# Kernel optimization log

Measured on AMD Instinct MI355X. Metric: run time of the kernel, lower is better.

Reference implementation:

```python
import jax, jax.numpy as jnp
import numpy as np

MARGIN = 0.2
EPS = 1e-6  # torch.pairwise_distance adds eps to the difference before the norm


def setup_inputs() -> dict:
    key = jax.random.key(0)
    k1, k2, k3 = jax.random.split(key, 3)
    B, D = 8192, 128
    emb1 = jax.random.normal(k1, (B, D), dtype=jnp.float32)
    emb2 = jax.random.normal(k2, (B, D), dtype=jnp.float32)
    target = jax.random.randint(k3, (B,), 0, 2, dtype=jnp.int64)
    return {"emb1": emb1, "emb2": emb2, "target": target}


def reference(emb1, emb2, target):
    B, D = emb1.shape
    # torch.pairwise_distance(a, b) = ||a - b + EPS||_2; expand the square:
    # |a-b+eps|^2 = |a|^2 + |b|^2 - 2 a.b + 2*eps*(sum(a)-sum(b)) + D*eps^2
    sq = (
        jnp.sum(emb1 * emb1, axis=-1)[:, None]
        + jnp.sum(emb2 * emb2, axis=-1)[None, :]
        - 2.0 * (emb1 @ emb2.T)
        + 2.0 * EPS * (jnp.sum(emb1, axis=-1)[:, None] - jnp.sum(emb2, axis=-1)[None, :])
        + D * EPS * EPS
    )
    dist = jnp.sqrt(jnp.maximum(sq, 0.0))  # [B, B]: dist[i, j] = ||emb1[i] - emb2[j] + eps||

    pos = target == 1
    neg = target == 0
    # hardest positive: max over columns j with target[j]==1; hardest negative: min over target[j]==0
    pos_max = jnp.max(jnp.where(pos[None, :], dist, -jnp.inf), axis=1)  # [B]
    neg_min = jnp.min(jnp.where(neg[None, :], dist, jnp.inf), axis=1)   # [B]
    per_anchor = jnp.maximum(pos_max - neg_min + MARGIN, 0.0)
    anchor_w = pos.astype(dist.dtype)
    # mean over anchors (rows i with target[i]==1)
    return jnp.sum(per_anchor * anchor_w) / jnp.sum(anchor_w)
```

## Files before the change

### kernel.cpp

```cpp
#include <hip/hip_runtime.h>
#include <hip/hip_bf16.h>
#include <math.h>


#define DDIM   128
#define SPLITS 8
#define MARGIN 0.2f
#define EPS    1e-6f
#define SENT   1e30f

#define CHUNK_PITCH 1056
#define WAVE_SPAN   (8 * CHUNK_PITCH)
#define TILE_BYTES  (4 * WAVE_SPAN)

typedef unsigned short ushort_t;
typedef __attribute__((ext_vector_type(8))) short short8;
typedef __attribute__((ext_vector_type(4))) float f32x4;

__device__ __forceinline__ ushort_t f2bf(float f) {
    unsigned int u = __float_as_uint(f);
    u = (u + 0x7FFFu + ((u >> 16) & 1u)) >> 16;
    return (ushort_t)u;
}

__device__ __forceinline__ void g2lds16(const ushort_t* g, void* lds) {
    __builtin_amdgcn_global_load_lds(
        (const __attribute__((address_space(1))) unsigned int*)g,
        (__attribute__((address_space(3))) unsigned int*)lds,
        16, 0, 0);
}

__global__ void prep_kernel(const float* __restrict__ e1, const float* __restrict__ e2,
                            const int* __restrict__ target,
                            ushort_t* __restrict__ e1b, ushort_t* __restrict__ e2b,
                            float* __restrict__ rowterm,
                            float* __restrict__ cpos, float* __restrict__ cneg,
                            float* __restrict__ redsum, int* __restrict__ ticket, int B) {
    if (blockIdx.x == 0 && threadIdx.x == 0) {
        redsum[0] = 0.f; redsum[1] = 0.f; *ticket = 0;
    }
    int w    = (blockIdx.x * blockDim.x + threadIdx.x) >> 6;
    int lane = threadIdx.x & 63;
    if (w >= 2 * B) return;
    bool first = (w < B);
    int r = first ? w : w - B;
    const float* src = (first ? e1 : e2) + (size_t)r * DDIM;
    float2 v = *(const float2*)(src + lane * 2);
    ushort_t* dst = (first ? e1b : e2b) + (size_t)r * DDIM;
    ushort2 o; o.x = f2bf(v.x); o.y = f2bf(v.y);
    *(ushort2*)(dst + lane * 2) = o;
    float s = v.x + v.y;
    float n = v.x * v.x + v.y * v.y;
    #pragma unroll
    for (int off = 32; off > 0; off >>= 1) {
        s += __shfl_down(s, off, 64);
        n += __shfl_down(n, off, 64);
    }
    if (lane == 0) {
        if (first) {
            rowterm[r] = n + 2.f * EPS * s + (float)DDIM * EPS * EPS;
        } else {
            float ct = n - 2.f * EPS * s;
            int tg = target[r];
            cpos[r] = (tg == 1) ? ct : -SENT;
            cneg[r] = (tg == 0) ? ct :  SENT;
        }
    }
}

__global__ __launch_bounds__(256, 2)
void tile_kernel(const ushort_t* __restrict__ e1b, const ushort_t* __restrict__ e2b,
                 const float* __restrict__ cpos, const float* __restrict__ cneg,
                 float* __restrict__ pmp, float* __restrict__ nmp, int B) {
    __shared__ __align__(16) unsigned char Bs[2][TILE_BYTES];
    __shared__ float smP[128], smN[128];

    const int tid = threadIdx.x;
    const int w   = tid >> 6;
    const int l   = tid & 63;
    const int lq  = l >> 4;
    const int lm  = l & 15;
    const int row0 = blockIdx.x * 128;
    const int colSpan = B / SPLITS;
    const int col0 = blockIdx.y * colSpan;
    const int nTiles = colSpan / 128;

    const int wr = (w >> 1) * 64;
    const int wc = (w & 1) * 64;

    auto stageB = [&](int t, int buf) {
        const ushort_t* g = e2b + (size_t)(col0 + t * 128 + w * 32) * DDIM + l * 8;
        unsigned char* lp = Bs[buf] + w * WAVE_SPAN;
        #pragma unroll
        for (int it = 0; it < 8; ++it)
            g2lds16(g + it * 512, lp + it * CHUNK_PITCH);
    };

    stageB(0, 0);

    short8 afr[4][4];
    {
        const ushort_t* aG = e1b + (size_t)(row0 + wr + lm) * DDIM + lq * 8;
        #pragma unroll
        for (int i = 0; i < 4; ++i)
            #pragma unroll
            for (int k4 = 0; k4 < 4; ++k4)
                afr[i][k4] = *(const short8*)(aG + i * 16 * DDIM + k4 * 32);
    }

    const int bOff = ((wc >> 2) + (lm >> 2)) * CHUNK_PITCH + (lm & 3) * 256 + lq * 16;

    float pm[4][4], nm[4][4];
    #pragma unroll
    for (int i = 0; i < 4; ++i)
        #pragma unroll
        for (int r = 0; r < 4; ++r) { pm[i][r] = -SENT; nm[i][r] = SENT; }

    __syncthreads();

    for (int t = 0; t < nTiles; ++t) {
        if (t + 1 < nTiles) stageB(t + 1, (t + 1) & 1);

        const unsigned char* bLane = Bs[t & 1] + bOff;

        f32x4 acc[4][4];
        #pragma unroll
        for (int i = 0; i < 4; ++i)
            #pragma unroll
            for (int j = 0; j < 4; ++j)
                acc[i][j] = (f32x4){0.f, 0.f, 0.f, 0.f};

        #pragma unroll
        for (int kk = 0; kk < DDIM; kk += 32) {
            const int k4 = kk >> 5;
            const int ko = kk * 2;
            short8 bf[4];
            #pragma unroll
            for (int j = 0; j < 4; ++j)
                bf[j] = *(const short8*)(bLane + j * (4 * CHUNK_PITCH) + ko);
            #pragma unroll
            for (int i = 0; i < 4; ++i)
                #pragma unroll
                for (int j = 0; j < 4; ++j)
                    acc[i][j] = __builtin_amdgcn_mfma_f32_16x16x32_bf16(
                                    afr[i][k4], bf[j], acc[i][j], 0, 0, 0);
        }

        #pragma unroll
        for (int j = 0; j < 4; ++j) {
            int col = col0 + t * 128 + wc + j * 16 + lm;
            float cp = cpos[col];
            float cn = cneg[col];
            #pragma unroll
            for (int i = 0; i < 4; ++i)
                #pragma unroll
                for (int r = 0; r < 4; ++r) {
                    float d = acc[i][j][r];
                    pm[i][r] = fmaxf(pm[i][r], fmaf(-2.f, d, cp));
                    nm[i][r] = fminf(nm[i][r], fmaf(-2.f, d, cn));
                }
        }

        if (t + 1 < nTiles)
            __syncthreads();
    }

    #pragma unroll
    for (int m = 1; m < 16; m <<= 1) {
        #pragma unroll
        for (int i = 0; i < 4; ++i)
            #pragma unroll
            for (int r = 0; r < 4; ++r) {
                pm[i][r] = fmaxf(pm[i][r], __shfl_xor(pm[i][r], m, 64));
                nm[i][r] = fminf(nm[i][r], __shfl_xor(nm[i][r], m, 64));
            }
    }

    __syncthreads();
    if ((w & 1) == 1 && lm == 0) {
        #pragma unroll
        for (int i = 0; i < 4; ++i)
            #pragma unroll
            for (int r = 0; r < 4; ++r) {
                int lr = wr + i * 16 + lq * 4 + r;
                smP[lr] = pm[i][r];
                smN[lr] = nm[i][r];
            }
    }
    __syncthreads();
    if ((w & 1) == 0 && lm == 0) {
        #pragma unroll
        for (int i = 0; i < 4; ++i)
            #pragma unroll
            for (int r = 0; r < 4; ++r) {
                int lr  = wr + i * 16 + lq * 4 + r;
                int row = row0 + lr;
                pmp[(size_t)blockIdx.y * B + row] = fmaxf(pm[i][r], smP[lr]);
                nmp[(size_t)blockIdx.y * B + row] = fminf(nm[i][r], smN[lr]);
            }
    }
}

__global__ void reduce_kernel(const float* __restrict__ pmp, const float* __restrict__ nmp,
                              const float* __restrict__ rowterm, const int* __restrict__ target,
                              float* __restrict__ redsum, int* __restrict__ ticket,
                              float* __restrict__ out, int B) {
    int row = blockIdx.x * blockDim.x + threadIdx.x;
    float s = 0.f, c = 0.f;
    {
        float pmv = -SENT, nmv = SENT;
        #pragma unroll
        for (int sp = 0; sp < SPLITS; ++sp) {
            pmv = fmaxf(pmv, pmp[(size_t)sp * B + row]);
            nmv = fminf(nmv, nmp[(size_t)sp * B + row]);
        }
        float rt = rowterm[row];
        float dp = sqrtf(fmaxf(rt + pmv, 0.f));
        float dn = sqrtf(fmaxf(rt + nmv, 0.f));
        if (target[row] == 1) {
            s = fmaxf(dp - dn + MARGIN, 0.f);
            c = 1.f;
        }
    }
    #pragma unroll
    for (int off = 32; off > 0; off >>= 1) {
        s += __shfl_down(s, off, 64);
        c += __shfl_down(c, off, 64);
    }
    __shared__ float ls[4], lc[4];
    int wv = threadIdx.x >> 6, ln = threadIdx.x & 63;
    if (ln == 0) { ls[wv] = s; lc[wv] = c; }
    __syncthreads();
    if (threadIdx.x == 0) {
        float ss = ls[0] + ls[1] + ls[2] + ls[3];
        float cc = lc[0] + lc[1] + lc[2] + lc[3];
        atomicAdd(&redsum[0], ss);
        atomicAdd(&redsum[1], cc);
        __threadfence();
        int done = atomicAdd(ticket, 1);
        if (done == (int)gridDim.x - 1) {
            __threadfence();
            float fs = __hip_atomic_load(&redsum[0], __ATOMIC_RELAXED, __HIP_MEMORY_SCOPE_AGENT);
            float fc = __hip_atomic_load(&redsum[1], __ATOMIC_RELAXED, __HIP_MEMORY_SCOPE_AGENT);
            out[0] = fs / fc;
        }
    }
}

extern "C" void kernel_launch(void* const* d_in, const int* in_sizes, int n_in,
                              void* d_out, int out_size, void* d_ws, size_t ws_size,
                              hipStream_t stream) {
    const float* e1     = (const float*)d_in[0];
    const float* e2     = (const float*)d_in[1];
    const int*   target = (const int*)d_in[2];
    float* out = (float*)d_out;
    const int B = in_sizes[2];

    char* p = (char*)d_ws;
    ushort_t* e1b  = (ushort_t*)p;   p += (size_t)B * DDIM * 2;
    ushort_t* e2b  = (ushort_t*)p;   p += (size_t)B * DDIM * 2;
    float* rowterm = (float*)p;      p += (size_t)B * 4;
    float* cpos    = (float*)p;      p += (size_t)B * 4;
    float* cneg    = (float*)p;      p += (size_t)B * 4;
    float* pmp     = (float*)p;      p += (size_t)SPLITS * B * 4;
    float* nmp     = (float*)p;      p += (size_t)SPLITS * B * 4;
    float* redsum  = (float*)p;      p += 2 * 4;
    int*   ticket  = (int*)p;

    {
        int blocks = (2 * B + 3) / 4;
        prep_kernel<<<blocks, 256, 0, stream>>>(e1, e2, target, e1b, e2b,
                                                rowterm, cpos, cneg, redsum, ticket, B);
    }
    {
        dim3 grid(B / 128, SPLITS);
        tile_kernel<<<grid, 256, 0, stream>>>(e1b, e2b, cpos, cneg, pmp, nmp, B);
    }
    reduce_kernel<<<32, 256, 0, stream>>>(pmp, nmp, rowterm, target,
                                          redsum, ticket, out, B);
}
```

Measured before the change: 92.09 us.

## Fuse final reduction into tile kernel via atomic max keys and last-block ticket

Replaces the per-split partial max/min buffers and separate reduce kernel with order-preserving uint-encoded atomicMax updates per row, then lets the last finishing tile block compute the final loss. This removes one kernel launch and the partial-buffer round trip. It adds global atomics per row, a serial single-block final reduction over all B rows, and fences in every block.

```diff
diff --git a/kernel.cpp b/kernel.cpp
--- a/kernel.cpp
+++ b/kernel.cpp
@@ -23,6 +23,15 @@
     return (ushort_t)u;
 }
 
+__device__ __forceinline__ unsigned enc(float f) {
+    unsigned b = __float_as_uint(f);
+    return (b & 0x80000000u) ? ~b : (b | 0x80000000u);
+}
+__device__ __forceinline__ float dec(unsigned k) {
+    unsigned b = (k & 0x80000000u) ? (k & 0x7FFFFFFFu) : ~k;
+    return __uint_as_float(b);
+}
+
 __device__ __forceinline__ void g2lds16(const ushort_t* g, void* lds) {
     __builtin_amdgcn_global_load_lds(
         (const __attribute__((address_space(1))) unsigned int*)g,
@@ -35,11 +44,13 @@
                             ushort_t* __restrict__ e1b, ushort_t* __restrict__ e2b,
                             float* __restrict__ rowterm,
                             float* __restrict__ cpos, float* __restrict__ cneg,
-                            float* __restrict__ redsum, int* __restrict__ ticket, int B) {
-    if (blockIdx.x == 0 && threadIdx.x == 0) {
-        redsum[0] = 0.f; redsum[1] = 0.f; *ticket = 0;
-    }
-    int w    = (blockIdx.x * blockDim.x + threadIdx.x) >> 6;
+                            unsigned* __restrict__ pmkey, unsigned* __restrict__ nmkey,
+                            int* __restrict__ ticket, int B) {
+    int gtid = blockIdx.x * blockDim.x + threadIdx.x;
+    if (gtid < B) { pmkey[gtid] = 0u; nmkey[gtid] = 0u; }
+    if (gtid == 0) *ticket = 0;
+
+    int w    = gtid >> 6;
     int lane = threadIdx.x & 63;
     if (w >= 2 * B) return;
     bool first = (w < B);
@@ -71,9 +82,12 @@
 __global__ __launch_bounds__(256, 2)
 void tile_kernel(const ushort_t* __restrict__ e1b, const ushort_t* __restrict__ e2b,
                  const float* __restrict__ cpos, const float* __restrict__ cneg,
-                 float* __restrict__ pmp, float* __restrict__ nmp, int B) {
-    __shared__ __align__(16) unsigned char Bs[2][TILE_BYTES];
+                 const float* __restrict__ rowterm, const int* __restrict__ target,
+                 unsigned* __restrict__ pmkey, unsigned* __restrict__ nmkey,
+                 int* __restrict__ ticket, float* __restrict__ out, int B) {
+    __shared__ __align__(16) unsigned char Bsm[2][TILE_BYTES];
     __shared__ float smP[128], smN[128];
+    __shared__ int lastSh;
 
     const int tid = threadIdx.x;
     const int w   = tid >> 6;
@@ -84,13 +98,14 @@
     const int colSpan = B / SPLITS;
     const int col0 = blockIdx.y * colSpan;
     const int nTiles = colSpan / 128;
+    const int nBlocks = gridDim.x * gridDim.y;
 
     const int wr = (w >> 1) * 64;
     const int wc = (w & 1) * 64;
 
     auto stageB = [&](int t, int buf) {
         const ushort_t* g = e2b + (size_t)(col0 + t * 128 + w * 32) * DDIM + l * 8;
-        unsigned char* lp = Bs[buf] + w * WAVE_SPAN;
+        unsigned char* lp = Bsm[buf] + w * WAVE_SPAN;
         #pragma unroll
         for (int it = 0; it < 8; ++it)
             g2lds16(g + it * 512, lp + it * CHUNK_PITCH);
@@ -121,7 +136,7 @@
     for (int t = 0; t < nTiles; ++t) {
         if (t + 1 < nTiles) stageB(t + 1, (t + 1) & 1);
 
-        const unsigned char* bLane = Bs[t & 1] + bOff;
+        const unsigned char* bLane = Bsm[t & 1] + bOff;
 
         f32x4 acc[4][4];
         #pragma unroll
@@ -161,8 +176,7 @@
                 }
         }
 
-        if (t + 1 < nTiles)
-            __syncthreads();
+        if (t + 1 < nTiles) __syncthreads();
     }
 
     #pragma unroll
@@ -195,55 +209,48 @@
             for (int r = 0; r < 4; ++r) {
                 int lr  = wr + i * 16 + lq * 4 + r;
                 int row = row0 + lr;
-                pmp[(size_t)blockIdx.y * B + row] = fmaxf(pm[i][r], smP[lr]);
-                nmp[(size_t)blockIdx.y * B + row] = fminf(nm[i][r], smN[lr]);
-            }
-    }
-}
-
-__global__ void reduce_kernel(const float* __restrict__ pmp, const float* __restrict__ nmp,
-                              const float* __restrict__ rowterm, const int* __restrict__ target,
-                              float* __restrict__ redsum, int* __restrict__ ticket,
-                              float* __restrict__ out, int B) {
-    int row = blockIdx.x * blockDim.x + threadIdx.x;
-    float s = 0.f, c = 0.f;
-    {
-        float pmv = -SENT, nmv = SENT;
-        #pragma unroll
-        for (int sp = 0; sp < SPLITS; ++sp) {
-            pmv = fmaxf(pmv, pmp[(size_t)sp * B + row]);
-            nmv = fminf(nmv, nmp[(size_t)sp * B + row]);
-        }
-        float rt = rowterm[row];
-        float dp = sqrtf(fmaxf(rt + pmv, 0.f));
-        float dn = sqrtf(fmaxf(rt + nmv, 0.f));
-        if (target[row] == 1) {
-            s = fmaxf(dp - dn + MARGIN, 0.f);
-            c = 1.f;
-        }
-    }
-    #pragma unroll
-    for (int off = 32; off > 0; off >>= 1) {
-        s += __shfl_down(s, off, 64);
-        c += __shfl_down(c, off, 64);
-    }
-    __shared__ float ls[4], lc[4];
-    int wv = threadIdx.x >> 6, ln = threadIdx.x & 63;
-    if (ln == 0) { ls[wv] = s; lc[wv] = c; }
-    __syncthreads();
-    if (threadIdx.x == 0) {
-        float ss = ls[0] + ls[1] + ls[2] + ls[3];
-        float cc = lc[0] + lc[1] + lc[2] + lc[3];
-        atomicAdd(&redsum[0], ss);
-        atomicAdd(&redsum[1], cc);
+                float p = fmaxf(pm[i][r], smP[lr]);
+                float n = fminf(nm[i][r], smN[lr]);
+                atomicMax(&pmkey[row], enc(p));
+                atomicMax(&nmkey[row], enc(-n));
+            }
+    }
+
+    __threadfence();
+    __syncthreads();
+    if (tid == 0) {
+        int done = atomicAdd(ticket, 1);
+        lastSh = (done == nBlocks - 1);
+    }
+    __syncthreads();
+    if (lastSh) {
         __threadfence();
-        int done = atomicAdd(ticket, 1);
-        if (done == (int)gridDim.x - 1) {
-            __threadfence();
-            float fs = __hip_atomic_load(&redsum[0], __ATOMIC_RELAXED, __HIP_MEMORY_SCOPE_AGENT);
-            float fc = __hip_atomic_load(&redsum[1], __ATOMIC_RELAXED, __HIP_MEMORY_SCOPE_AGENT);
-            out[0] = fs / fc;
-        }
+        float s = 0.f, c = 0.f;
+        for (int row = tid; row < B; row += 256) {
+            unsigned kp = __hip_atomic_load(&pmkey[row], __ATOMIC_RELAXED,
+                                            __HIP_MEMORY_SCOPE_AGENT);
+            unsigned kn = __hip_atomic_load(&nmkey[row], __ATOMIC_RELAXED,
+                                            __HIP_MEMORY_SCOPE_AGENT);
+            float rt  = rowterm[row];
+            float pmv = dec(kp);
+            float nmv = -dec(kn);
+            float dp = sqrtf(fmaxf(rt + pmv, 0.f));
+            float dn = sqrtf(fmaxf(rt + nmv, 0.f));
+            if (target[row] == 1) {
+                s += fmaxf(dp - dn + MARGIN, 0.f);
+                c += 1.f;
+            }
+        }
+        #pragma unroll
+        for (int off = 32; off > 0; off >>= 1) {
+            s += __shfl_down(s, off, 64);
+            c += __shfl_down(c, off, 64);
+        }
+        if (l == 0) { smP[w] = s; smN[w] = c; }
+        __syncthreads();
+        if (tid == 0)
+            out[0] = (smP[0] + smP[1] + smP[2] + smP[3])
+                   / (smN[0] + smN[1] + smN[2] + smN[3]);
     }
 }
 
@@ -257,25 +264,25 @@
     const int B = in_sizes[2];
 
     char* p = (char*)d_ws;
-    ushort_t* e1b  = (ushort_t*)p;   p += (size_t)B * DDIM * 2;
-    ushort_t* e2b  = (ushort_t*)p;   p += (size_t)B * DDIM * 2;
-    float* rowterm = (float*)p;      p += (size_t)B * 4;
-    float* cpos    = (float*)p;      p += (size_t)B * 4;
-    float* cneg    = (float*)p;      p += (size_t)B * 4;
-    float* pmp     = (float*)p;      p += (size_t)SPLITS * B * 4;
-    float* nmp     = (float*)p;      p += (size_t)SPLITS * B * 4;
-    float* redsum  = (float*)p;      p += 2 * 4;
-    int*   ticket  = (int*)p;
+    ushort_t* e1b     = (ushort_t*)p;  p += (size_t)B * DDIM * 2;
+    ushort_t* e2b     = (ushort_t*)p;  p += (size_t)B * DDIM * 2;
+    float*    rowterm = (float*)p;     p += (size_t)B * 4;
+    float*    cpos    = (float*)p;     p += (size_t)B * 4;
+    float*    cneg    = (float*)p;     p += (size_t)B * 4;
+    unsigned* pmkey   = (unsigned*)p;  p += (size_t)B * 4;
+    unsigned* nmkey   = (unsigned*)p;  p += (size_t)B * 4;
+    int*      ticket  = (int*)p;
 
     {
         int blocks = (2 * B + 3) / 4;
         prep_kernel<<<blocks, 256, 0, stream>>>(e1, e2, target, e1b, e2b,
-                                                rowterm, cpos, cneg, redsum, ticket, B);
+                                                rowterm, cpos, cneg,
+                                                pmkey, nmkey, ticket, B);
     }
     {
         dim3 grid(B / 128, SPLITS);
-        tile_kernel<<<grid, 256, 0, stream>>>(e1b, e2b, cpos, cneg, pmp, nmp, B);
-    }
-    reduce_kernel<<<32, 256, 0, stream>>>(pmp, nmp, rowterm, target,
-                                          redsum, ticket, out, B);
-}
+        tile_kernel<<<grid, 256, 0, stream>>>(e1b, e2b, cpos, cneg,
+                                              rowterm, target,
+                                              pmkey, nmkey, ticket, out, B);
+    }
+}
```

Result: slower. 128.6 us (+39.6%).
